# Kernel tuning notes

Hardware: AMD Instinct MI355X
Metric: run time of the kernel (lower is better)

The kernel has to match this reference:

```python
import jax, jax.numpy as jnp
import numpy as np

H = W = 32
CROP = int(H * 0.8)  # 25, matches int(H*crop_ratio) in torch
MEAN = jnp.array([0.5071, 0.4867, 0.4408], jnp.float32).reshape(1, 3, 1, 1)
STD = jnp.array([0.2675, 0.2565, 0.2761], jnp.float32).reshape(1, 3, 1, 1)


def _bilinear(img, iy, ix):
    # img [C,H,W]; iy/ix [H,W] float pixel coords (reflected+clamped already)
    y0 = jnp.floor(iy); x0 = jnp.floor(ix)
    wy = iy - y0; wx = ix - x0
    y0i = jnp.clip(y0.astype(jnp.int32), 0, H - 1); y1i = jnp.clip(y0i + 1, 0, H - 1)
    x0i = jnp.clip(x0.astype(jnp.int32), 0, W - 1); x1i = jnp.clip(x0i + 1, 0, W - 1)
    v00 = img[:, y0i, x0i]; v01 = img[:, y0i, x1i]
    v10 = img[:, y1i, x0i]; v11 = img[:, y1i, x1i]
    return v00 * (1 - wy) * (1 - wx) + v01 * (1 - wy) * wx + v10 * wy * (1 - wx) + v11 * wy * wx


def _reflect(c, size):
    # PyTorch grid_sample reflection padding, align_corners=False (reflect about -0.5 / size-0.5)
    lo = -0.5
    span = float(size)
    t = jnp.abs(c - lo)
    extra = jnp.mod(t, span)
    flips = jnp.floor(t / span)
    out = jnp.where(jnp.mod(flips, 2.0) == 0.0, lo + extra, lo + span - extra)
    return jnp.clip(out, 0.0, size - 1.0)


def _crop_resize_one(img, top, left):
    # bilinear resize of img[:, top:top+CROP, left:left+CROP] -> HxW, align_corners=False
    d = (jnp.arange(W, dtype=jnp.float32) + 0.5) * (CROP / W) - 0.5
    d = jnp.maximum(d, 0.0)
    i0 = jnp.floor(d).astype(jnp.int32)
    lam = d - i0
    i1 = jnp.minimum(i0 + 1, CROP - 1)
    r0 = top + i0; r1 = top + i1; c0 = left + i0; c1 = left + i1
    v00 = img[:, r0[:, None], c0[None, :]]
    v01 = img[:, r0[:, None], c1[None, :]]
    v10 = img[:, r1[:, None], c0[None, :]]
    v11 = img[:, r1[:, None], c1[None, :]]
    ly = lam[:, None]; lx = lam[None, :]
    return v00 * (1 - ly) * (1 - lx) + v01 * (1 - ly) * lx + v10 * ly * (1 - lx) + v11 * ly * lx


def _grid_sample_one(img, theta):
    # affine_grid + grid_sample (bilinear, reflection, align_corners=False)
    xs = (2.0 * (jnp.arange(W, dtype=jnp.float32) + 0.5) / W) - 1.0
    ys = (2.0 * (jnp.arange(H, dtype=jnp.float32) + 0.5) / H) - 1.0
    yn, xn = jnp.meshgrid(ys, xs, indexing='ij')
    gx = theta[0, 0] * xn + theta[0, 1] * yn + theta[0, 2]
    gy = theta[1, 0] * xn + theta[1, 1] * yn + theta[1, 2]
    ix = _reflect(((gx + 1.0) * W - 1.0) * 0.5, W)
    iy = _reflect(((gy + 1.0) * H - 1.0) * 0.5, H)
    return _bilinear(img, iy, ix)


def _augment(x, shared_affine, apply_crop):
    B = x.shape[0]
    ks = jax.random.split(jax.random.key(42), 10)
    x = x * STD + MEAN  # de-normalize
    if apply_crop:
        max_off = H - CROP
        top = jax.random.randint(ks[0], (B,), 0, max_off + 1)
        left = jax.random.randint(ks[1], (B,), 0, max_off + 1)
        x = jax.vmap(_crop_resize_one)(x, top, left)
    flip_mask = jax.random.uniform(ks[2], (B,)) < 0.5
    x = jnp.where(flip_mask[:, None, None, None], x[..., ::-1], x)
    # shared affine is provided -> always applied (torch shared_affine branch)
    x = jax.vmap(_grid_sample_one)(x, shared_affine)
    brightness = 1.0 + (jax.random.uniform(ks[3], (B, 1, 1, 1)) - 0.5) * 0.8
    x = x * brightness
    gray = x.mean(axis=1, keepdims=True)
    contrast = 1.0 + (jax.random.uniform(ks[4], (B, 1, 1, 1)) - 0.5) * 0.8
    x = gray + (x - gray) * contrast
    gray = x.mean(axis=1, keepdims=True)
    saturation = 1.0 + (jax.random.uniform(ks[5], (B, 1, 1, 1)) - 0.5) * 0.8
    x = gray + (x - gray) * saturation
    hue_mask = jax.random.uniform(ks[6], (B,)) < 0.5
    x = jnp.where(hue_mask[:, None, None, None], x[:, ::-1], x)  # BGR swap
    gray_mask = jax.random.uniform(ks[7], (B,)) < 0.2
    x = jnp.where(gray_mask[:, None, None, None], x.mean(axis=1, keepdims=True), x)
    blur_mask = jax.random.uniform(ks[8], (B,)) < 0.5
    xp = jnp.pad(x, ((0, 0), (0, 0), (1, 1), (1, 1)), mode='edge')  # replicate pad
    bl = sum(xp[:, :, i:i + H, j:j + W] for i in range(3) for j in range(3)) / 9.0  # 3x3 box blur
    x = jnp.where(blur_mask[:, None, None, None], bl, x)
    solar_mask = jax.random.uniform(ks[9], (B,)) < 0.1
    x = jnp.where(solar_mask[:, None, None, None] & (x > 0.5), 1.0 - x, x)
    x = jnp.clip(x, 0.0, 1.0)
    x = (x - MEAN) / STD  # re-normalize
    return x, flip_mask


def setup_inputs() -> dict:
    key = jax.random.key(0)
    k1, k2 = jax.random.split(key)
    B = 8192
    x = jax.random.normal(k1, (B, 3, H, W), jnp.float32)
    eye = jnp.broadcast_to(jnp.array([[1.0, 0.0, 0.0], [0.0, 1.0, 0.0]], jnp.float32), (B, 2, 3))
    shared_affine = eye + 0.1 * jax.random.normal(k2, (B, 2, 3), jnp.float32)
    return {"x": x, "shared_affine": shared_affine, "apply_crop": 1}


def reference(x, shared_affine, apply_crop):
    out, flip_mask = _augment(x, shared_affine, int(apply_crop))
    # torch returns (x, {'flip': flip_mask, 'affine': affine_theta})
    return out, flip_mask, shared_affine
```

## Files before the change

kernel.cpp:

```cpp
#include <hip/hip_runtime.h>

#define HW 32
#define NPIX 1024
#define IMG 3072

__device__ __forceinline__ unsigned rotl32(unsigned x, int d) {
    return (x << d) | (x >> (32 - d));
}

struct UPair { unsigned a, b; };

__device__ __forceinline__ UPair threefry2x32(unsigned k0, unsigned k1,
                                              unsigned x0, unsigned x1) {
    unsigned k2 = k0 ^ k1 ^ 0x1BD11BDAu;
    x0 += k0; x1 += k1;
#define RND(r) { x0 += x1; x1 = rotl32(x1, (r)); x1 ^= x0; }
    RND(13) RND(15) RND(26) RND(6)
    x0 += k1; x1 += k2 + 1u;
    RND(17) RND(29) RND(16) RND(24)
    x0 += k2; x1 += k0 + 2u;
    RND(13) RND(15) RND(26) RND(6)
    x0 += k0; x1 += k1 + 3u;
    RND(17) RND(29) RND(16) RND(24)
    x0 += k1; x1 += k2 + 4u;
    RND(13) RND(15) RND(26) RND(6)
    x0 += k2; x1 += k0 + 5u;
#undef RND
    return {x0, x1};
}

__device__ __forceinline__ float bits_to_u01(unsigned bits) {
    return __uint_as_float((bits >> 9) | 0x3f800000u) - 1.0f;
}

__device__ __forceinline__ float reflect32(float c) {
    float t = fabsf(c + 0.5f);
    float extra = fmodf(t, 32.0f);
    float flips = floorf(t * 0.03125f);
    float par = fmodf(flips, 2.0f);
    float o = (par == 0.0f) ? (extra - 0.5f) : (31.5f - extra);
    return fminf(fmaxf(o, 0.0f), 31.0f);
}

__global__ __launch_bounds__(256) void aug_kernel(
    const float* __restrict__ xin, const float* __restrict__ aff,
    const int* __restrict__ apply_crop, float* __restrict__ out, int B) {
    __shared__ __align__(16) float bufA[IMG];
    __shared__ __align__(16) float bufB[IMG];
    __shared__ float s_theta[6];
    __shared__ int s_top, s_left, s_flip, s_hue, s_gray, s_blur, s_solar;
    __shared__ float s_bright, s_contr, s_sat;

    const int b = blockIdx.x;
    const int t = threadIdx.x;
    const bool do_crop = (apply_crop[0] != 0);

    const float MEANc[3] = {0.5071f, 0.4867f, 0.4408f};
    const float STDc[3]  = {0.2675f, 0.2565f, 0.2761f};
    const float INVSTD[3] = {1.0f / 0.2675f, 1.0f / 0.2565f, 1.0f / 0.2761f};

    const float4* imgv = (const float4*)(xin + (size_t)b * IMG);
    float4 ld0 = imgv[t];
    float4 ld1 = imgv[t + 256];
    float4 ld2 = imgv[t + 512];

    const size_t OUT_IMG = (size_t)B * IMG;
    if (t < 6) {
        float v = aff[b * 6 + t];
        s_theta[t] = v;
        out[OUT_IMG + (size_t)B + (size_t)b * 6 + t] = v;
    }

    if (t < 10) {
        int k = t;
        UPair K = threefry2x32(0u, 42u, 0u, (unsigned)k);
        if (k < 2) {
            UPair k2 = threefry2x32(K.a, K.b, 0u, 1u);
            UPair r = threefry2x32(k2.a, k2.b, 0u, (unsigned)b);
            int val = (int)((r.a ^ r.b) & 7u);
            if (k == 0) s_top = val; else s_left = val;
        } else {
            UPair r = threefry2x32(K.a, K.b, 0u, (unsigned)b);
            float u = bits_to_u01(r.a ^ r.b);
            if      (k == 2) s_flip  = (u < 0.5f);
            else if (k == 3) s_bright = 1.0f + (u - 0.5f) * 0.8f;
            else if (k == 4) s_contr  = 1.0f + (u - 0.5f) * 0.8f;
            else if (k == 5) s_sat    = 1.0f + (u - 0.5f) * 0.8f;
            else if (k == 6) s_hue   = (u < 0.5f);
            else if (k == 7) s_gray  = (u < 0.2f);
            else if (k == 8) s_blur  = (u < 0.5f);
            else             s_solar = (u < 0.1f);
        }
    }

    {
        float4 v = ld0;
        v.x = v.x * STDc[0] + MEANc[0]; v.y = v.y * STDc[0] + MEANc[0];
        v.z = v.z * STDc[0] + MEANc[0]; v.w = v.w * STDc[0] + MEANc[0];
        ((float4*)bufA)[t] = v;
        v = ld1;
        v.x = v.x * STDc[1] + MEANc[1]; v.y = v.y * STDc[1] + MEANc[1];
        v.z = v.z * STDc[1] + MEANc[1]; v.w = v.w * STDc[1] + MEANc[1];
        ((float4*)bufA)[t + 256] = v;
        v = ld2;
        v.x = v.x * STDc[2] + MEANc[2]; v.y = v.y * STDc[2] + MEANc[2];
        v.z = v.z * STDc[2] + MEANc[2]; v.w = v.w * STDc[2] + MEANc[2];
        ((float4*)bufA)[t + 512] = v;
    }
    __syncthreads();

    if (t == 0) out[OUT_IMG + b] = s_flip ? 1.0f : 0.0f;

    float* cur = bufA;
    float* nxt = bufB;

    if (do_crop) {
        const int top = s_top, left = s_left;
#pragma unroll
        for (int m = 0; m < 4; ++m) {
            int s = t + 256 * m;
            int yi = s >> 5, xj = s & 31;
            float di = fmaxf(((float)yi + 0.5f) * 0.78125f - 0.5f, 0.0f);
            float dj = fmaxf(((float)xj + 0.5f) * 0.78125f - 0.5f, 0.0f);
            int i0 = (int)di; float ly = di - (float)i0; int i1 = min(i0 + 1, 24);
            int q0 = (int)dj; float lx = dj - (float)q0; int q1 = min(q0 + 1, 24);
            int r0 = (top + i0) * HW, r1 = (top + i1) * HW;
            int c0 = left + q0, c1 = left + q1;
            float w00 = (1.0f - ly) * (1.0f - lx), w01 = (1.0f - ly) * lx;
            float w10 = ly * (1.0f - lx), w11 = ly * lx;
#pragma unroll
            for (int c = 0; c < 3; ++c) {
                const float* p = cur + c * NPIX;
                nxt[c * NPIX + s] = p[r0 + c0] * w00 + p[r0 + c1] * w01 +
                                    p[r1 + c0] * w10 + p[r1 + c1] * w11;
            }
        }
        float* tp = cur; cur = nxt; nxt = tp;
        __syncthreads();
    }

    {
        const int flip = s_flip, hue = s_hue, grayf = s_gray;
        const float br = s_bright, ct = s_contr, sa = s_sat;
        const float th0 = s_theta[0], th1 = s_theta[1], th2 = s_theta[2];
        const float th3 = s_theta[3], th4 = s_theta[4], th5 = s_theta[5];
#pragma unroll
        for (int m = 0; m < 4; ++m) {
            int s = t + 256 * m;
            int yi = s >> 5, xj = s & 31;
            float xn = ((float)xj + 0.5f) * 0.0625f - 1.0f;
            float yn = ((float)yi + 0.5f) * 0.0625f - 1.0f;
            float gx = th0 * xn + th1 * yn + th2;
            float gy = th3 * xn + th4 * yn + th5;
            float ix = reflect32(((gx + 1.0f) * 32.0f - 1.0f) * 0.5f);
            float iy = reflect32(((gy + 1.0f) * 32.0f - 1.0f) * 0.5f);
            float fy = floorf(iy), fx = floorf(ix);
            float wy = iy - fy, wx = ix - fx;
            int y0 = min(max((int)fy, 0), 31); int y1 = min(y0 + 1, 31);
            int x0 = min(max((int)fx, 0), 31); int x1 = min(x0 + 1, 31);
            if (flip) { x0 = 31 - x0; x1 = 31 - x1; }
            int r0 = y0 * HW, r1 = y1 * HW;
            float w00 = (1.0f - wy) * (1.0f - wx), w01 = (1.0f - wy) * wx;
            float w10 = wy * (1.0f - wx), w11 = wy * wx;
            float ch0, ch1, ch2;
            {
                const float* p = cur;
                ch0 = p[r0 + x0] * w00 + p[r0 + x1] * w01 +
                      p[r1 + x0] * w10 + p[r1 + x1] * w11;
            }
            {
                const float* p = cur + NPIX;
                ch1 = p[r0 + x0] * w00 + p[r0 + x1] * w01 +
                      p[r1 + x0] * w10 + p[r1 + x1] * w11;
            }
            {
                const float* p = cur + 2 * NPIX;
                ch2 = p[r0 + x0] * w00 + p[r0 + x1] * w01 +
                      p[r1 + x0] * w10 + p[r1 + x1] * w11;
            }
            ch0 *= br; ch1 *= br; ch2 *= br;
            float g = (ch0 + ch1 + ch2) * (1.0f / 3.0f);
            ch0 = g + (ch0 - g) * ct; ch1 = g + (ch1 - g) * ct; ch2 = g + (ch2 - g) * ct;
            g = (ch0 + ch1 + ch2) * (1.0f / 3.0f);
            ch0 = g + (ch0 - g) * sa; ch1 = g + (ch1 - g) * sa; ch2 = g + (ch2 - g) * sa;
            if (hue) { float tmp = ch0; ch0 = ch2; ch2 = tmp; }
            if (grayf) { g = (ch0 + ch1 + ch2) * (1.0f / 3.0f); ch0 = ch1 = ch2 = g; }
            nxt[s] = ch0; nxt[NPIX + s] = ch1; nxt[2 * NPIX + s] = ch2;
        }
        float* tp = cur; cur = nxt; nxt = tp;
        __syncthreads();
    }

    {
        const int blur = s_blur, solar = s_solar;
        float* o = out + (size_t)b * IMG;
#pragma unroll
        for (int m = 0; m < 4; ++m) {
            int s = t + 256 * m;
            int yi = s >> 5, xj = s & 31;
            int ym = max(yi - 1, 0) * HW, yc = yi * HW, yp = min(yi + 1, 31) * HW;
            int xm = max(xj - 1, 0), xp = min(xj + 1, 31);
#pragma unroll
            for (int c = 0; c < 3; ++c) {
                const float* p = cur + c * NPIX;
                float v = p[yc + xj];
                float r = v;
                if (blur) {
                    float sum = p[ym + xm] + p[ym + xj] + p[ym + xp] +
                                p[yc + xm] + v          + p[yc + xp] +
                                p[yp + xm] + p[yp + xj] + p[yp + xp];
                    r = sum * (1.0f / 9.0f);
                }
                if (solar && r > 0.5f) r = 1.0f - r;
                r = fminf(fmaxf(r, 0.0f), 1.0f);
                r = (r - MEANc[c]) * INVSTD[c];
                o[c * NPIX + s] = r;
            }
        }
    }
}

extern "C" void kernel_launch(void* const* d_in, const int* in_sizes, int n_in,
                              void* d_out, int out_size, void* d_ws, size_t ws_size,
                              hipStream_t stream) {
    const float* x = (const float*)d_in[0];
    const float* aff = (const float*)d_in[1];
    const int* ac = (const int*)d_in[2];
    float* out = (float*)d_out;
    int B = in_sizes[0] / IMG;
    aug_kernel<<<dim3(B), dim3(256), 0, stream>>>(x, aff, ac, out, B);
}
```

Before: 181.7 us.

## Process four contiguous pixels per thread with vectorized LDS I/O and folded color math

Each thread now handles four adjacent pixels in one row rather than four strided ones. Per-row terms are computed once, LDS and global stores become float4, and the blur stage builds separable row sums from float4 plus edge loads. The brightness, contrast, saturation and grayscale chain is folded into two scalars K1 and K2, and the hue swap becomes a choice of store destination. The fmodf calls in the reflection are replaced by floor-based arithmetic. The aim is fewer instructions and wider memory ops, at the cost of more registers and possible LDS bank conflicts on the gathers and float4 accesses.

Result: slower. 196.2 us (+8.0%).

```diff
diff --git a/kernel.cpp b/kernel.cpp
--- a/kernel.cpp
+++ b/kernel.cpp
@@ -35,9 +35,9 @@
 
 __device__ __forceinline__ float reflect32(float c) {
     float t = fabsf(c + 0.5f);
-    float extra = fmodf(t, 32.0f);
-    float flips = floorf(t * 0.03125f);
-    float par = fmodf(flips, 2.0f);
+    float f = floorf(t * 0.03125f);
+    float extra = t - 32.0f * f;
+    float par = f - 2.0f * floorf(f * 0.5f);
     float o = (par == 0.0f) ? (extra - 0.5f) : (31.5f - extra);
     return fminf(fmaxf(o, 0.0f), 31.0f);
 }
@@ -59,10 +59,11 @@
     const float STDc[3]  = {0.2675f, 0.2565f, 0.2761f};
     const float INVSTD[3] = {1.0f / 0.2675f, 1.0f / 0.2565f, 1.0f / 0.2761f};
 
-    const float4* imgv = (const float4*)(xin + (size_t)b * IMG);
-    float4 ld0 = imgv[t];
-    float4 ld1 = imgv[t + 256];
-    float4 ld2 = imgv[t + 512];
+    const float* imgp = xin + (size_t)b * IMG;
+    const int p0 = 4 * t;
+    float4 g0 = *(const float4*)(imgp + p0);
+    float4 g1 = *(const float4*)(imgp + NPIX + p0);
+    float4 g2 = *(const float4*)(imgp + 2 * NPIX + p0);
 
     const size_t OUT_IMG = (size_t)B * IMG;
     if (t < 6) {
@@ -94,18 +95,18 @@
     }
 
     {
-        float4 v = ld0;
+        float4 v = g0;
         v.x = v.x * STDc[0] + MEANc[0]; v.y = v.y * STDc[0] + MEANc[0];
         v.z = v.z * STDc[0] + MEANc[0]; v.w = v.w * STDc[0] + MEANc[0];
-        ((float4*)bufA)[t] = v;
-        v = ld1;
+        *(float4*)(bufA + p0) = v;
+        v = g1;
         v.x = v.x * STDc[1] + MEANc[1]; v.y = v.y * STDc[1] + MEANc[1];
         v.z = v.z * STDc[1] + MEANc[1]; v.w = v.w * STDc[1] + MEANc[1];
-        ((float4*)bufA)[t + 256] = v;
-        v = ld2;
+        *(float4*)(bufA + NPIX + p0) = v;
+        v = g2;
         v.x = v.x * STDc[2] + MEANc[2]; v.y = v.y * STDc[2] + MEANc[2];
         v.z = v.z * STDc[2] + MEANc[2]; v.w = v.w * STDc[2] + MEANc[2];
-        ((float4*)bufA)[t + 512] = v;
+        *(float4*)(bufA + 2 * NPIX + p0) = v;
     }
     __syncthreads();
 
@@ -114,46 +115,57 @@
     float* cur = bufA;
     float* nxt = bufB;
 
+    const int yrow = p0 >> 5;
+    const int xcol = p0 & 31;
+
     if (do_crop) {
         const int top = s_top, left = s_left;
-#pragma unroll
-        for (int m = 0; m < 4; ++m) {
-            int s = t + 256 * m;
-            int yi = s >> 5, xj = s & 31;
-            float di = fmaxf(((float)yi + 0.5f) * 0.78125f - 0.5f, 0.0f);
-            float dj = fmaxf(((float)xj + 0.5f) * 0.78125f - 0.5f, 0.0f);
-            int i0 = (int)di; float ly = di - (float)i0; int i1 = min(i0 + 1, 24);
+        float di = fmaxf(((float)yrow + 0.5f) * 0.78125f - 0.5f, 0.0f);
+        int i0 = (int)di; float ly = di - (float)i0; int i1 = min(i0 + 1, 24);
+        int r0 = (top + i0) * HW, r1 = (top + i1) * HW;
+        float omy = 1.0f - ly;
+        float oc[3][4];
+#pragma unroll
+        for (int k = 0; k < 4; ++k) {
+            int x = xcol + k;
+            float dj = fmaxf(((float)x + 0.5f) * 0.78125f - 0.5f, 0.0f);
             int q0 = (int)dj; float lx = dj - (float)q0; int q1 = min(q0 + 1, 24);
-            int r0 = (top + i0) * HW, r1 = (top + i1) * HW;
             int c0 = left + q0, c1 = left + q1;
-            float w00 = (1.0f - ly) * (1.0f - lx), w01 = (1.0f - ly) * lx;
+            float w00 = omy * (1.0f - lx), w01 = omy * lx;
             float w10 = ly * (1.0f - lx), w11 = ly * lx;
+            int a00 = r0 + c0, a01 = r0 + c1, a10 = r1 + c0, a11 = r1 + c1;
 #pragma unroll
             for (int c = 0; c < 3; ++c) {
                 const float* p = cur + c * NPIX;
-                nxt[c * NPIX + s] = p[r0 + c0] * w00 + p[r0 + c1] * w01 +
-                                    p[r1 + c0] * w10 + p[r1 + c1] * w11;
+                oc[c][k] = p[a00] * w00 + p[a01] * w01 +
+                           p[a10] * w10 + p[a11] * w11;
             }
         }
+#pragma unroll
+        for (int c = 0; c < 3; ++c)
+            *(float4*)(nxt + c * NPIX + p0) =
+                make_float4(oc[c][0], oc[c][1], oc[c][2], oc[c][3]);
         float* tp = cur; cur = nxt; nxt = tp;
         __syncthreads();
     }
 
     {
         const int flip = s_flip, hue = s_hue, grayf = s_gray;
-        const float br = s_bright, ct = s_contr, sa = s_sat;
+        float K1 = s_bright * s_contr * s_sat;
+        float K2 = s_bright - K1;
+        if (grayf) { K1 = 0.0f; K2 = s_bright; }
         const float th0 = s_theta[0], th1 = s_theta[1], th2 = s_theta[2];
         const float th3 = s_theta[3], th4 = s_theta[4], th5 = s_theta[5];
-#pragma unroll
-        for (int m = 0; m < 4; ++m) {
-            int s = t + 256 * m;
-            int yi = s >> 5, xj = s & 31;
-            float xn = ((float)xj + 0.5f) * 0.0625f - 1.0f;
-            float yn = ((float)yi + 0.5f) * 0.0625f - 1.0f;
+        float yn = ((float)yrow + 0.5f) * 0.0625f - 1.0f;
+        float oc[3][4];
+#pragma unroll
+        for (int k = 0; k < 4; ++k) {
+            int x = xcol + k;
+            float xn = ((float)x + 0.5f) * 0.0625f - 1.0f;
             float gx = th0 * xn + th1 * yn + th2;
             float gy = th3 * xn + th4 * yn + th5;
-            float ix = reflect32(((gx + 1.0f) * 32.0f - 1.0f) * 0.5f);
-            float iy = reflect32(((gy + 1.0f) * 32.0f - 1.0f) * 0.5f);
+            float ix = reflect32((gx + 1.0f) * 16.0f - 0.5f);
+            float iy = reflect32((gy + 1.0f) * 16.0f - 0.5f);
             float fy = floorf(iy), fx = floorf(ix);
             float wy = iy - fy, wx = ix - fx;
             int y0 = min(max((int)fy, 0), 31); int y1 = min(y0 + 1, 31);
@@ -162,31 +174,26 @@
             int r0 = y0 * HW, r1 = y1 * HW;
             float w00 = (1.0f - wy) * (1.0f - wx), w01 = (1.0f - wy) * wx;
             float w10 = wy * (1.0f - wx), w11 = wy * wx;
-            float ch0, ch1, ch2;
-            {
-                const float* p = cur;
-                ch0 = p[r0 + x0] * w00 + p[r0 + x1] * w01 +
-                      p[r1 + x0] * w10 + p[r1 + x1] * w11;
-            }
-            {
-                const float* p = cur + NPIX;
-                ch1 = p[r0 + x0] * w00 + p[r0 + x1] * w01 +
-                      p[r1 + x0] * w10 + p[r1 + x1] * w11;
-            }
-            {
-                const float* p = cur + 2 * NPIX;
-                ch2 = p[r0 + x0] * w00 + p[r0 + x1] * w01 +
-                      p[r1 + x0] * w10 + p[r1 + x1] * w11;
-            }
-            ch0 *= br; ch1 *= br; ch2 *= br;
+            int a00 = r0 + x0, a01 = r0 + x1, a10 = r1 + x0, a11 = r1 + x1;
+            float ch0 = cur[a00] * w00 + cur[a01] * w01 +
+                        cur[a10] * w10 + cur[a11] * w11;
+            const float* p1 = cur + NPIX;
+            float ch1 = p1[a00] * w00 + p1[a01] * w01 +
+                        p1[a10] * w10 + p1[a11] * w11;
+            const float* p2 = cur + 2 * NPIX;
+            float ch2 = p2[a00] * w00 + p2[a01] * w01 +
+                        p2[a10] * w10 + p2[a11] * w11;
             float g = (ch0 + ch1 + ch2) * (1.0f / 3.0f);
-            ch0 = g + (ch0 - g) * ct; ch1 = g + (ch1 - g) * ct; ch2 = g + (ch2 - g) * ct;
-            g = (ch0 + ch1 + ch2) * (1.0f / 3.0f);
-            ch0 = g + (ch0 - g) * sa; ch1 = g + (ch1 - g) * sa; ch2 = g + (ch2 - g) * sa;
-            if (hue) { float tmp = ch0; ch0 = ch2; ch2 = tmp; }
-            if (grayf) { g = (ch0 + ch1 + ch2) * (1.0f / 3.0f); ch0 = ch1 = ch2 = g; }
-            nxt[s] = ch0; nxt[NPIX + s] = ch1; nxt[2 * NPIX + s] = ch2;
-        }
+            oc[0][k] = K1 * ch0 + K2 * g;
+            oc[1][k] = K1 * ch1 + K2 * g;
+            oc[2][k] = K1 * ch2 + K2 * g;
+        }
+        float* d0 = nxt + (hue ? 2 * NPIX : 0) + p0;
+        float* d2 = nxt + (hue ? 0 : 2 * NPIX) + p0;
+        *(float4*)d0 = make_float4(oc[0][0], oc[0][1], oc[0][2], oc[0][3]);
+        *(float4*)(nxt + NPIX + p0) =
+            make_float4(oc[1][0], oc[1][1], oc[1][2], oc[1][3]);
+        *(float4*)d2 = make_float4(oc[2][0], oc[2][1], oc[2][2], oc[2][3]);
         float* tp = cur; cur = nxt; nxt = tp;
         __syncthreads();
     }
@@ -194,28 +201,41 @@
     {
         const int blur = s_blur, solar = s_solar;
         float* o = out + (size_t)b * IMG;
-#pragma unroll
-        for (int m = 0; m < 4; ++m) {
-            int s = t + 256 * m;
-            int yi = s >> 5, xj = s & 31;
-            int ym = max(yi - 1, 0) * HW, yc = yi * HW, yp = min(yi + 1, 31) * HW;
-            int xm = max(xj - 1, 0), xp = min(xj + 1, 31);
-#pragma unroll
-            for (int c = 0; c < 3; ++c) {
-                const float* p = cur + c * NPIX;
-                float v = p[yc + xj];
-                float r = v;
-                if (blur) {
-                    float sum = p[ym + xm] + p[ym + xj] + p[ym + xp] +
-                                p[yc + xm] + v          + p[yc + xp] +
-                                p[yp + xm] + p[yp + xj] + p[yp + xp];
-                    r = sum * (1.0f / 9.0f);
-                }
-                if (solar && r > 0.5f) r = 1.0f - r;
-                r = fminf(fmaxf(r, 0.0f), 1.0f);
-                r = (r - MEANc[c]) * INVSTD[c];
-                o[c * NPIX + s] = r;
+        int ym = max(yrow - 1, 0) * HW, yc = yrow * HW, yp = min(yrow + 1, 31) * HW;
+        int xl = max(xcol - 1, 0), xr = min(xcol + 4, 31);
+#pragma unroll
+        for (int c = 0; c < 3; ++c) {
+            const float* p = cur + c * NPIX;
+            float4 m0 = *(const float4*)(p + ym + xcol);
+            float L0 = p[ym + xl], R0 = p[ym + xr];
+            float4 m1 = *(const float4*)(p + yc + xcol);
+            float L1 = p[yc + xl], R1 = p[yc + xr];
+            float4 m2 = *(const float4*)(p + yp + xcol);
+            float L2 = p[yp + xl], R2 = p[yp + xr];
+            float h0x = L0 + m0.x + m0.y, h0y = m0.x + m0.y + m0.z;
+            float h0z = m0.y + m0.z + m0.w, h0w = m0.z + m0.w + R0;
+            float h1x = L1 + m1.x + m1.y, h1y = m1.x + m1.y + m1.z;
+            float h1z = m1.y + m1.z + m1.w, h1w = m1.z + m1.w + R1;
+            float h2x = L2 + m2.x + m2.y, h2y = m2.x + m2.y + m2.z;
+            float h2z = m2.y + m2.z + m2.w, h2w = m2.z + m2.w + R2;
+            float sx = h0x + h1x + h2x, sy = h0y + h1y + h2y;
+            float sz = h0z + h1z + h2z, sw = h0w + h1w + h2w;
+            float4 r;
+            r.x = blur ? sx * (1.0f / 9.0f) : m1.x;
+            r.y = blur ? sy * (1.0f / 9.0f) : m1.y;
+            r.z = blur ? sz * (1.0f / 9.0f) : m1.z;
+            r.w = blur ? sw * (1.0f / 9.0f) : m1.w;
+            if (solar) {
+                r.x = (r.x > 0.5f) ? 1.0f - r.x : r.x;
+                r.y = (r.y > 0.5f) ? 1.0f - r.y : r.y;
+                r.z = (r.z > 0.5f) ? 1.0f - r.z : r.z;
+                r.w = (r.w > 0.5f) ? 1.0f - r.w : r.w;
             }
+            r.x = (fminf(fmaxf(r.x, 0.0f), 1.0f) - MEANc[c]) * INVSTD[c];
+            r.y = (fminf(fmaxf(r.y, 0.0f), 1.0f) - MEANc[c]) * INVSTD[c];
+            r.z = (fminf(fmaxf(r.z, 0.0f), 1.0f) - MEANc[c]) * INVSTD[c];
+            r.w = (fminf(fmaxf(r.w, 0.0f), 1.0f) - MEANc[c]) * INVSTD[c];
+            *(float4*)(o + c * NPIX + p0) = r;
         }
     }
 }
```

## Interleave channels in LDS as float4, fold color ops, separable blur

Applied to the files above, without the earlier changes.

Shared-memory image buffers switch from planar to pixel-interleaved float4 (RGB plus padding), so each bilinear tap reads all channels in a single LDS access. Brightness, contrast, saturation and grayscale are algebraically folded into two per-image coefficients. The 3x3 box blur becomes separable, with a horizontal pass through LDS followed by a vertical pass. The reflect function replaces fmodf with floor arithmetic. The change adds one barrier, uses more LDS per block and turns the global input loads into scalar loads.

Measured after the change: 194.6 us. 7.1% more time.

```diff
diff --git a/kernel.cpp b/kernel.cpp
--- a/kernel.cpp
+++ b/kernel.cpp
@@ -35,9 +35,9 @@
 
 __device__ __forceinline__ float reflect32(float c) {
     float t = fabsf(c + 0.5f);
-    float extra = fmodf(t, 32.0f);
-    float flips = floorf(t * 0.03125f);
-    float par = fmodf(flips, 2.0f);
+    float f = floorf(t * 0.03125f);
+    float extra = t - 32.0f * f;
+    float par = f - 2.0f * floorf(f * 0.5f);
     float o = (par == 0.0f) ? (extra - 0.5f) : (31.5f - extra);
     return fminf(fmaxf(o, 0.0f), 31.0f);
 }
@@ -45,8 +45,8 @@
 __global__ __launch_bounds__(256) void aug_kernel(
     const float* __restrict__ xin, const float* __restrict__ aff,
     const int* __restrict__ apply_crop, float* __restrict__ out, int B) {
-    __shared__ __align__(16) float bufA[IMG];
-    __shared__ __align__(16) float bufB[IMG];
+    __shared__ __align__(16) float bufA[NPIX * 4];
+    __shared__ __align__(16) float bufB[NPIX * 4];
     __shared__ float s_theta[6];
     __shared__ int s_top, s_left, s_flip, s_hue, s_gray, s_blur, s_solar;
     __shared__ float s_bright, s_contr, s_sat;
@@ -55,14 +55,22 @@
     const int t = threadIdx.x;
     const bool do_crop = (apply_crop[0] != 0);
 
+    const int x = t & 31;
+    const int ybase = t >> 5;
+
     const float MEANc[3] = {0.5071f, 0.4867f, 0.4408f};
     const float STDc[3]  = {0.2675f, 0.2565f, 0.2761f};
     const float INVSTD[3] = {1.0f / 0.2675f, 1.0f / 0.2565f, 1.0f / 0.2761f};
 
-    const float4* imgv = (const float4*)(xin + (size_t)b * IMG);
-    float4 ld0 = imgv[t];
-    float4 ld1 = imgv[t + 256];
-    float4 ld2 = imgv[t + 512];
+    const float* imgp = xin + (size_t)b * IMG;
+    float l0[4], l1[4], l2[4];
+#pragma unroll
+    for (int m = 0; m < 4; ++m) {
+        int s = t + 256 * m;
+        l0[m] = imgp[s];
+        l1[m] = imgp[NPIX + s];
+        l2[m] = imgp[2 * NPIX + s];
+    }
 
     const size_t OUT_IMG = (size_t)B * IMG;
     if (t < 6) {
@@ -93,19 +101,13 @@
         }
     }
 
-    {
-        float4 v = ld0;
-        v.x = v.x * STDc[0] + MEANc[0]; v.y = v.y * STDc[0] + MEANc[0];
-        v.z = v.z * STDc[0] + MEANc[0]; v.w = v.w * STDc[0] + MEANc[0];
-        ((float4*)bufA)[t] = v;
-        v = ld1;
-        v.x = v.x * STDc[1] + MEANc[1]; v.y = v.y * STDc[1] + MEANc[1];
-        v.z = v.z * STDc[1] + MEANc[1]; v.w = v.w * STDc[1] + MEANc[1];
-        ((float4*)bufA)[t + 256] = v;
-        v = ld2;
-        v.x = v.x * STDc[2] + MEANc[2]; v.y = v.y * STDc[2] + MEANc[2];
-        v.z = v.z * STDc[2] + MEANc[2]; v.w = v.w * STDc[2] + MEANc[2];
-        ((float4*)bufA)[t + 512] = v;
+#pragma unroll
+    for (int m = 0; m < 4; ++m) {
+        int s = t + 256 * m;
+        *(float4*)(bufA + 4 * s) = make_float4(
+            l0[m] * STDc[0] + MEANc[0],
+            l1[m] * STDc[1] + MEANc[1],
+            l2[m] * STDc[2] + MEANc[2], 0.0f);
     }
     __syncthreads();
 
@@ -116,44 +118,54 @@
 
     if (do_crop) {
         const int top = s_top, left = s_left;
-#pragma unroll
-        for (int m = 0; m < 4; ++m) {
-            int s = t + 256 * m;
-            int yi = s >> 5, xj = s & 31;
-            float di = fmaxf(((float)yi + 0.5f) * 0.78125f - 0.5f, 0.0f);
-            float dj = fmaxf(((float)xj + 0.5f) * 0.78125f - 0.5f, 0.0f);
+        float dj = fmaxf(((float)x + 0.5f) * 0.78125f - 0.5f, 0.0f);
+        int q0 = (int)dj; float lx = dj - (float)q0; int q1 = min(q0 + 1, 24);
+        int c0 = left + q0, c1 = left + q1;
+        float omx = 1.0f - lx;
+#pragma unroll
+        for (int m = 0; m < 4; ++m) {
+            int y = ybase + 8 * m;
+            int s = y * HW + x;
+            float di = fmaxf(((float)y + 0.5f) * 0.78125f - 0.5f, 0.0f);
             int i0 = (int)di; float ly = di - (float)i0; int i1 = min(i0 + 1, 24);
-            int q0 = (int)dj; float lx = dj - (float)q0; int q1 = min(q0 + 1, 24);
             int r0 = (top + i0) * HW, r1 = (top + i1) * HW;
-            int c0 = left + q0, c1 = left + q1;
-            float w00 = (1.0f - ly) * (1.0f - lx), w01 = (1.0f - ly) * lx;
-            float w10 = ly * (1.0f - lx), w11 = ly * lx;
-#pragma unroll
-            for (int c = 0; c < 3; ++c) {
-                const float* p = cur + c * NPIX;
-                nxt[c * NPIX + s] = p[r0 + c0] * w00 + p[r0 + c1] * w01 +
-                                    p[r1 + c0] * w10 + p[r1 + c1] * w11;
-            }
+            float w00 = (1.0f - ly) * omx, w01 = (1.0f - ly) * lx;
+            float w10 = ly * omx, w11 = ly * lx;
+            float4 v00 = *(const float4*)(cur + 4 * (r0 + c0));
+            float4 v01 = *(const float4*)(cur + 4 * (r0 + c1));
+            float4 v10 = *(const float4*)(cur + 4 * (r1 + c0));
+            float4 v11 = *(const float4*)(cur + 4 * (r1 + c1));
+            float4 r;
+            r.x = v00.x * w00 + v01.x * w01 + v10.x * w10 + v11.x * w11;
+            r.y = v00.y * w00 + v01.y * w01 + v10.y * w10 + v11.y * w11;
+            r.z = v00.z * w00 + v01.z * w01 + v10.z * w10 + v11.z * w11;
+            r.w = 0.0f;
+            *(float4*)(nxt + 4 * s) = r;
         }
         float* tp = cur; cur = nxt; nxt = tp;
         __syncthreads();
     }
 
+    float4 own[4];
     {
         const int flip = s_flip, hue = s_hue, grayf = s_gray;
-        const float br = s_bright, ct = s_contr, sa = s_sat;
+        float K1 = s_bright * s_contr * s_sat;
+        float K2 = s_bright - K1;
+        if (grayf) { K1 = 0.0f; K2 = s_bright; }
         const float th0 = s_theta[0], th1 = s_theta[1], th2 = s_theta[2];
         const float th3 = s_theta[3], th4 = s_theta[4], th5 = s_theta[5];
-#pragma unroll
-        for (int m = 0; m < 4; ++m) {
-            int s = t + 256 * m;
-            int yi = s >> 5, xj = s & 31;
-            float xn = ((float)xj + 0.5f) * 0.0625f - 1.0f;
-            float yn = ((float)yi + 0.5f) * 0.0625f - 1.0f;
-            float gx = th0 * xn + th1 * yn + th2;
-            float gy = th3 * xn + th4 * yn + th5;
-            float ix = reflect32(((gx + 1.0f) * 32.0f - 1.0f) * 0.5f);
-            float iy = reflect32(((gy + 1.0f) * 32.0f - 1.0f) * 0.5f);
+        const float xn = ((float)x + 0.5f) * 0.0625f - 1.0f;
+        const float gx0 = th0 * xn + th2;
+        const float gy0 = th3 * xn + th5;
+#pragma unroll
+        for (int m = 0; m < 4; ++m) {
+            int y = ybase + 8 * m;
+            int s = y * HW + x;
+            float yn = ((float)y + 0.5f) * 0.0625f - 1.0f;
+            float gx = gx0 + th1 * yn;
+            float gy = gy0 + th4 * yn;
+            float ix = reflect32((gx + 1.0f) * 16.0f - 0.5f);
+            float iy = reflect32((gy + 1.0f) * 16.0f - 0.5f);
             float fy = floorf(iy), fx = floorf(ix);
             float wy = iy - fy, wx = ix - fx;
             int y0 = min(max((int)fy, 0), 31); int y1 = min(y0 + 1, 31);
@@ -162,60 +174,78 @@
             int r0 = y0 * HW, r1 = y1 * HW;
             float w00 = (1.0f - wy) * (1.0f - wx), w01 = (1.0f - wy) * wx;
             float w10 = wy * (1.0f - wx), w11 = wy * wx;
-            float ch0, ch1, ch2;
-            {
-                const float* p = cur;
-                ch0 = p[r0 + x0] * w00 + p[r0 + x1] * w01 +
-                      p[r1 + x0] * w10 + p[r1 + x1] * w11;
-            }
-            {
-                const float* p = cur + NPIX;
-                ch1 = p[r0 + x0] * w00 + p[r0 + x1] * w01 +
-                      p[r1 + x0] * w10 + p[r1 + x1] * w11;
-            }
-            {
-                const float* p = cur + 2 * NPIX;
-                ch2 = p[r0 + x0] * w00 + p[r0 + x1] * w01 +
-                      p[r1 + x0] * w10 + p[r1 + x1] * w11;
-            }
-            ch0 *= br; ch1 *= br; ch2 *= br;
+            float4 v00 = *(const float4*)(cur + 4 * (r0 + x0));
+            float4 v01 = *(const float4*)(cur + 4 * (r0 + x1));
+            float4 v10 = *(const float4*)(cur + 4 * (r1 + x0));
+            float4 v11 = *(const float4*)(cur + 4 * (r1 + x1));
+            float ch0 = v00.x * w00 + v01.x * w01 + v10.x * w10 + v11.x * w11;
+            float ch1 = v00.y * w00 + v01.y * w01 + v10.y * w10 + v11.y * w11;
+            float ch2 = v00.z * w00 + v01.z * w01 + v10.z * w10 + v11.z * w11;
             float g = (ch0 + ch1 + ch2) * (1.0f / 3.0f);
-            ch0 = g + (ch0 - g) * ct; ch1 = g + (ch1 - g) * ct; ch2 = g + (ch2 - g) * ct;
-            g = (ch0 + ch1 + ch2) * (1.0f / 3.0f);
-            ch0 = g + (ch0 - g) * sa; ch1 = g + (ch1 - g) * sa; ch2 = g + (ch2 - g) * sa;
-            if (hue) { float tmp = ch0; ch0 = ch2; ch2 = tmp; }
-            if (grayf) { g = (ch0 + ch1 + ch2) * (1.0f / 3.0f); ch0 = ch1 = ch2 = g; }
-            nxt[s] = ch0; nxt[NPIX + s] = ch1; nxt[2 * NPIX + s] = ch2;
+            float o0 = K1 * ch0 + K2 * g;
+            float o1 = K1 * ch1 + K2 * g;
+            float o2 = K1 * ch2 + K2 * g;
+            if (hue) { float tmp = o0; o0 = o2; o2 = tmp; }
+            float4 r = make_float4(o0, o1, o2, 0.0f);
+            own[m] = r;
         }
         float* tp = cur; cur = nxt; nxt = tp;
+#pragma unroll
+        for (int m = 0; m < 4; ++m) {
+            int s = (ybase + 8 * m) * HW + x;
+            *(float4*)(cur + 4 * s) = own[m];
+        }
+        __syncthreads();
+    }
+
+    float4 hsum[4];
+    {
+        const int xl = max(x - 1, 0), xr = min(x + 1, 31);
+#pragma unroll
+        for (int m = 0; m < 4; ++m) {
+            int row = (ybase + 8 * m) * HW;
+            float4 vl = *(const float4*)(cur + 4 * (row + xl));
+            float4 vr = *(const float4*)(cur + 4 * (row + xr));
+            float4 h;
+            h.x = vl.x + own[m].x + vr.x;
+            h.y = vl.y + own[m].y + vr.y;
+            h.z = vl.z + own[m].z + vr.z;
+            h.w = 0.0f;
+            hsum[m] = h;
+        }
+#pragma unroll
+        for (int m = 0; m < 4; ++m) {
+            int s = (ybase + 8 * m) * HW + x;
+            *(float4*)(nxt + 4 * s) = hsum[m];
+        }
         __syncthreads();
     }
 
     {
         const int blur = s_blur, solar = s_solar;
         float* o = out + (size_t)b * IMG;
-#pragma unroll
-        for (int m = 0; m < 4; ++m) {
-            int s = t + 256 * m;
-            int yi = s >> 5, xj = s & 31;
-            int ym = max(yi - 1, 0) * HW, yc = yi * HW, yp = min(yi + 1, 31) * HW;
-            int xm = max(xj - 1, 0), xp = min(xj + 1, 31);
-#pragma unroll
-            for (int c = 0; c < 3; ++c) {
-                const float* p = cur + c * NPIX;
-                float v = p[yc + xj];
-                float r = v;
-                if (blur) {
-                    float sum = p[ym + xm] + p[ym + xj] + p[ym + xp] +
-                                p[yc + xm] + v          + p[yc + xp] +
-                                p[yp + xm] + p[yp + xj] + p[yp + xp];
-                    r = sum * (1.0f / 9.0f);
-                }
-                if (solar && r > 0.5f) r = 1.0f - r;
-                r = fminf(fmaxf(r, 0.0f), 1.0f);
-                r = (r - MEANc[c]) * INVSTD[c];
-                o[c * NPIX + s] = r;
+        const float* hb = nxt;
+#pragma unroll
+        for (int m = 0; m < 4; ++m) {
+            int y = ybase + 8 * m;
+            int s = y * HW + x;
+            int ym = max(y - 1, 0) * HW + x, yp = min(y + 1, 31) * HW + x;
+            float4 hu = *(const float4*)(hb + 4 * ym);
+            float4 hd = *(const float4*)(hb + 4 * yp);
+            float r0 = blur ? (hu.x + hsum[m].x + hd.x) * (1.0f / 9.0f) : own[m].x;
+            float r1 = blur ? (hu.y + hsum[m].y + hd.y) * (1.0f / 9.0f) : own[m].y;
+            float r2 = blur ? (hu.z + hsum[m].z + hd.z) * (1.0f / 9.0f) : own[m].z;
+            if (solar) {
+                r0 = (r0 > 0.5f) ? 1.0f - r0 : r0;
+                r1 = (r1 > 0.5f) ? 1.0f - r1 : r1;
+                r2 = (r2 > 0.5f) ? 1.0f - r2 : r2;
             }
+            r0 = (fminf(fmaxf(r0, 0.0f), 1.0f) - MEANc[0]) * INVSTD[0];
+            r1 = (fminf(fmaxf(r1, 0.0f), 1.0f) - MEANc[1]) * INVSTD[1];
+            r2 = (fminf(fmaxf(r2, 0.0f), 1.0f) - MEANc[2]) * INVSTD[2];
+            o[s] = r0;
+            o[NPIX + s] = r1;
+            o[2 * NPIX + s] = r2;
         }
     }
 }
```
